# Performance work log

Hardware: AMD Instinct MI355X
Metric: run time of the kernel (lower is better)

The kernel has to match this reference:

```python
import jax, jax.numpy as jnp
import numpy as np

B, S, E = 2, 8192, 128


def setup_inputs() -> dict:
    key = jax.random.key(0)
    ks = jax.random.split(key, 7)
    sc = 1.0 / np.sqrt(E)
    return {
        "x": jax.random.normal(ks[0], (B, S, E), dtype=jnp.float32),
        "Wq": jax.random.normal(ks[1], (E, E), dtype=jnp.float32) * sc,
        "bq": jax.random.normal(ks[2], (E,), dtype=jnp.float32) * 0.01,
        "Wk": jax.random.normal(ks[3], (E, E), dtype=jnp.float32) * sc,
        "bk": jax.random.normal(ks[4], (E,), dtype=jnp.float32) * 0.01,
        "Wv": jax.random.normal(ks[5], (E, E), dtype=jnp.float32) * sc,
        "bv": jax.random.normal(ks[6], (E,), dtype=jnp.float32) * 0.01,
    }


def reference(x, Wq, bq, Wk, bk, Wv, bv):
    # x: [B, S, E]. Conv1d(k=1) == per-slice linear: out[b,s,o] = sum_e W[o,e] x[b,s,e] + b[o]
    embed_dim = x.shape[-1]
    Q = jnp.einsum("bse,oe->bso", x, Wq) + bq  # [B, S, E]
    K = jnp.einsum("bse,oe->bso", x, Wk) + bk
    V = jnp.einsum("bse,oe->bso", x, Wv) + bv
    scores = jnp.einsum("bsd,btd->bst", Q, K) / jnp.sqrt(
        jnp.asarray(embed_dim, dtype=x.dtype)
    )  # [B, S, S]
    A = jax.nn.softmax(scores, axis=-1)
    # torch: out = bmm(V^T_as[B,E,S], A^T)[.transpose] == sum_t A[b,s,t] V[b,t,e]
    out = jnp.einsum("bst,bte->bse", A, V)  # [B, S, E]
    return out
```

## Files before the change

kernel.cpp:

```cpp
#include <hip/hip_runtime.h>
#include <math.h>

#define NB 2
#define NS 8192
#define NE 128
#define NROWS (NB * NS)

typedef __attribute__((ext_vector_type(8))) short s8v;
typedef __attribute__((ext_vector_type(16))) float fx16;
typedef __attribute__((ext_vector_type(2))) unsigned int u2v;
typedef __attribute__((address_space(1))) const unsigned char as1c;
typedef __attribute__((address_space(3))) unsigned char as3t;

static __device__ __forceinline__ unsigned int pkbf(float a, float b) {
    unsigned int ua = __float_as_uint(a), ub = __float_as_uint(b);
    ua += 0x7FFFu + ((ua >> 16) & 1u);
    ub += 0x7FFFu + ((ub >> 16) & 1u);
    return (ua >> 16) | (ub & 0xFFFF0000u);
}

static __device__ __forceinline__ unsigned int cvtpk(float a, float b) {
    unsigned int r;
    asm("v_cvt_pk_bf16_f32 %0, %1, %2" : "=v"(r) : "v"(a), "v"(b));
    return r;
}

__global__ __launch_bounds__(256, 2)
void qkv_kernel(const float* __restrict__ x,
                const float* __restrict__ Wq, const float* __restrict__ bq,
                const float* __restrict__ Wk, const float* __restrict__ bk,
                const float* __restrict__ Wv, const float* __restrict__ bv,
                unsigned short* __restrict__ qkv)
{
    __shared__ unsigned short WhL[64 * 136];
    __shared__ unsigned short WlL[64 * 136];

    const int t    = threadIdx.x;
    const int rblk = blockIdx.x * 128;
    const int mat  = blockIdx.y;
    const int o0   = blockIdx.z * 64;

    const float* W    = (mat == 0) ? Wq : (mat == 1) ? Wk : Wv;
    const float* bias = (mat == 0) ? bq : (mat == 1) ? bk : bv;
    unsigned short* out = qkv + (size_t)mat * NROWS * NE;
    const float osc = (mat == 0) ? 0.1275174460620886f : 1.0f;

    {
        const int r = t >> 2, cg = (t & 3) * 32;
        #pragma unroll
        for (int j = 0; j < 4; ++j) {
            const float* wp = &W[(size_t)(o0 + r) * NE + cg + j * 8];
            float4 a = *(const float4*)wp;
            float4 b = *(const float4*)(wp + 4);
            unsigned int h0 = pkbf(a.x, a.y), h1 = pkbf(a.z, a.w);
            unsigned int h2 = pkbf(b.x, b.y), h3 = pkbf(b.z, b.w);
            *(uint4*)&WhL[r * 136 + cg + j * 8] = make_uint4(h0, h1, h2, h3);
            float l0 = a.x - __uint_as_float(h0 << 16);
            float l1 = a.y - __uint_as_float(h0 & 0xFFFF0000u);
            float l2 = a.z - __uint_as_float(h1 << 16);
            float l3 = a.w - __uint_as_float(h1 & 0xFFFF0000u);
            float l4 = b.x - __uint_as_float(h2 << 16);
            float l5 = b.y - __uint_as_float(h2 & 0xFFFF0000u);
            float l6 = b.z - __uint_as_float(h3 << 16);
            float l7 = b.w - __uint_as_float(h3 & 0xFFFF0000u);
            *(uint4*)&WlL[r * 136 + cg + j * 8] =
                make_uint4(pkbf(l0, l1), pkbf(l2, l3), pkbf(l4, l5), pkbf(l6, l7));
        }
    }
    __syncthreads();

    const int w = t >> 6, lane = t & 63, lq = lane & 31, h = lane >> 5;
    const int rw = rblk + w * 32;

    s8v xhf[8], xlf[8];
    #pragma unroll
    for (int s = 0; s < 8; ++s) {
        const float* xp = &x[(size_t)(rw + lq) * NE + s * 16 + h * 8];
        float4 a = *(const float4*)xp;
        float4 b = *(const float4*)(xp + 4);
        unsigned int h0 = pkbf(a.x, a.y), h1 = pkbf(a.z, a.w);
        unsigned int h2 = pkbf(b.x, b.y), h3 = pkbf(b.z, b.w);
        float l0 = a.x - __uint_as_float(h0 << 16);
        float l1 = a.y - __uint_as_float(h0 & 0xFFFF0000u);
        float l2 = a.z - __uint_as_float(h1 << 16);
        float l3 = a.w - __uint_as_float(h1 & 0xFFFF0000u);
        float l4 = b.x - __uint_as_float(h2 << 16);
        float l5 = b.y - __uint_as_float(h2 & 0xFFFF0000u);
        float l6 = b.z - __uint_as_float(h3 << 16);
        float l7 = b.w - __uint_as_float(h3 & 0xFFFF0000u);
        union { uint4 u; s8v v; } H, L;
        H.u = make_uint4(h0, h1, h2, h3);
        L.u = make_uint4(pkbf(l0, l1), pkbf(l2, l3), pkbf(l4, l5), pkbf(l6, l7));
        xhf[s] = H.v;
        xlf[s] = L.v;
    }

    fx16 acc[2];
    #pragma unroll
    for (int ot = 0; ot < 2; ++ot)
        #pragma unroll
        for (int i = 0; i < 16; ++i) acc[ot][i] = 0.f;

    #pragma unroll
    for (int s = 0; s < 8; ++s) {
        #pragma unroll
        for (int ot = 0; ot < 2; ++ot) {
            s8v wh = *(const s8v*)&WhL[(ot * 32 + lq) * 136 + s * 16 + h * 8];
            s8v wl = *(const s8v*)&WlL[(ot * 32 + lq) * 136 + s * 16 + h * 8];
            if (mat != 2) {
                acc[ot] = __builtin_amdgcn_mfma_f32_32x32x16_bf16(wh, xhf[s], acc[ot], 0, 0, 0);
                acc[ot] = __builtin_amdgcn_mfma_f32_32x32x16_bf16(wh, xlf[s], acc[ot], 0, 0, 0);
                acc[ot] = __builtin_amdgcn_mfma_f32_32x32x16_bf16(wl, xhf[s], acc[ot], 0, 0, 0);
            } else {
                acc[ot] = __builtin_amdgcn_mfma_f32_32x32x16_bf16(xhf[s], wh, acc[ot], 0, 0, 0);
                acc[ot] = __builtin_amdgcn_mfma_f32_32x32x16_bf16(xlf[s], wh, acc[ot], 0, 0, 0);
                acc[ot] = __builtin_amdgcn_mfma_f32_32x32x16_bf16(xhf[s], wl, acc[ot], 0, 0, 0);
            }
        }
    }

    if (mat != 2) {
        const size_t rbase = (size_t)(rw + lq) * NE;
        #pragma unroll
        for (int ot = 0; ot < 2; ++ot)
            #pragma unroll
            for (int g = 0; g < 4; ++g) {
                int ob = o0 + ot * 32 + 4 * h + 8 * g;
                float4 bb = *(const float4*)&bias[ob];
                float v0 = (acc[ot][4 * g + 0] + bb.x) * osc;
                float v1 = (acc[ot][4 * g + 1] + bb.y) * osc;
                float v2 = (acc[ot][4 * g + 2] + bb.z) * osc;
                float v3 = (acc[ot][4 * g + 3] + bb.w) * osc;
                *(uint2*)&out[rbase + ob] = make_uint2(pkbf(v0, v1), pkbf(v2, v3));
            }
    } else {
        const int bb_ = rw >> 13, kb = (rw & (NS - 1)) + 4 * h;
        #pragma unroll
        for (int ot = 0; ot < 2; ++ot) {
            int o = o0 + ot * 32 + lq;
            float bv = bias[o];
            size_t obase = ((size_t)(bb_ * NE + o) << 13) + kb;
            #pragma unroll
            for (int g = 0; g < 4; ++g) {
                float v0 = acc[ot][4 * g + 0] + bv;
                float v1 = acc[ot][4 * g + 1] + bv;
                float v2 = acc[ot][4 * g + 2] + bv;
                float v3 = acc[ot][4 * g + 3] + bv;
                *(uint2*)&out[obase + 8 * g] = make_uint2(pkbf(v0, v1), pkbf(v2, v3));
            }
        }
    }
}

__global__ __launch_bounds__(256, 2)
void attn_kernel(const unsigned short* __restrict__ qkv,
                 _Float16* __restrict__ pd,
                 _Float16* __restrict__ pw,
                 float* __restrict__ ml)
{
    __shared__ unsigned short kbuf[2][64 * 128];
    __shared__ unsigned short vbuf[2][64 * 128];

    const int t  = threadIdx.x;
    const int id = blockIdx.x;
    const int ks = id & 3;
    const int b  = (id >> 2) & 1;
    const int T  = id >> 3;

    const unsigned short* Qg = qkv;
    const unsigned short* Kg = qkv + (size_t)NROWS * NE;
    const unsigned short* Vb = qkv + (size_t)2 * NROWS * NE + ((size_t)b << 20);

    const int w = t >> 6, lane = t & 63, lq = lane & 31, h = lane >> 5;
    const int qbw = b * NS + T * 128 + w * 32;
    const size_t kvb = (size_t)b * NS * NE;
    const int kq0 = ks * 2048;

    s8v qf[8];
    #pragma unroll
    for (int s = 0; s < 8; ++s)
        qf[s] = *(const s8v*)(Qg + (size_t)(qbw + lq) * NE + s * 16 + h * 8);

    fx16 acc[4];
    #pragma unroll
    for (int dt = 0; dt < 4; ++dt)
        #pragma unroll
        for (int i = 0; i < 16; ++i) acc[dt][i] = 0.f;

    float l = 0.f;

    const unsigned short* gptr[8];
    if (w < 2) {
        #pragma unroll
        for (int j = 0; j < 8; ++j) {
            int i = 8 * w + j;
            int keyl = 4 * i + (lane >> 4);
            int c = (lane & 15) ^ (keyl & 7);
            gptr[j] = Kg + kvb + (size_t)(kq0 + keyl) * NE + c * 8;
        }
    } else {
        #pragma unroll
        for (int j = 0; j < 8; ++j) {
            int i = 8 * (w - 2) + j;
            int d = 8 * i + (lane >> 3);
            int g = (lane & 7) ^ (d & 7);
            gptr[j] = Vb + ((size_t)d << 13) + kq0 + g * 8;
        }
    }
    const int gstride = (w < 2) ? 64 * NE : 64;

    auto stage = [&](int bufi) {
        if (w < 2) {
            #pragma unroll
            for (int j = 0; j < 8; ++j) {
                __builtin_amdgcn_global_load_lds((as1c*)gptr[j],
                    (as3t*)&kbuf[bufi][(8 * w + j) * 512], 16, 0, 0);
                gptr[j] += gstride;
            }
        } else {
            #pragma unroll
            for (int j = 0; j < 8; ++j) {
                __builtin_amdgcn_global_load_lds((as1c*)gptr[j],
                    (as3t*)&vbuf[bufi][(8 * (w - 2) + j) * 512], 16, 0, 0);
                gptr[j] += gstride;
            }
        }
    };

    stage(0);
    __syncthreads();

#define PEX(i) (st2[(i) >> 4][(i) & 15])
    int buf = 0;
    const int swz = (lq & 7) * 8;

    for (int r = 0; r < 32; ++r) {
        if (r < 31) stage(buf ^ 1);

        fx16 st2[2];
        #pragma unroll
        for (int mt = 0; mt < 2; ++mt)
            #pragma unroll
            for (int i = 0; i < 16; ++i) st2[mt][i] = 0.f;
        __builtin_amdgcn_s_setprio(1);
        #pragma unroll
        for (int s = 0; s < 8; ++s) {
            int co = ((s * 2 + h) * 8) ^ swz;
            s8v a0 = *(const s8v*)&kbuf[buf][lq * 128 + co];
            s8v a1 = *(const s8v*)&kbuf[buf][(32 + lq) * 128 + co];
            st2[0] = __builtin_amdgcn_mfma_f32_32x32x16_bf16(a0, qf[s], st2[0], 0, 0, 0);
            st2[1] = __builtin_amdgcn_mfma_f32_32x32x16_bf16(a1, qf[s], st2[1], 0, 0, 0);
        }
        __builtin_amdgcn_s_setprio(0);

        float a0s = 0.f, a1s = 0.f, a2s = 0.f, a3s = 0.f;
        #pragma unroll
        for (int i = 0; i < 32; i += 4) {
            PEX(i)     = __builtin_amdgcn_exp2f(PEX(i));
            PEX(i + 1) = __builtin_amdgcn_exp2f(PEX(i + 1));
            PEX(i + 2) = __builtin_amdgcn_exp2f(PEX(i + 2));
            PEX(i + 3) = __builtin_amdgcn_exp2f(PEX(i + 3));
            a0s += PEX(i); a1s += PEX(i + 1); a2s += PEX(i + 2); a3s += PEX(i + 3);
        }
        float lsum = (a0s + a1s) + (a2s + a3s);
        lsum += __shfl_xor(lsum, 32);
        l += lsum;

        #pragma unroll
        for (int s2 = 0; s2 < 4; ++s2) {
            unsigned int P0 = cvtpk(PEX(s2 * 8 + 0), PEX(s2 * 8 + 1));
            unsigned int P1 = cvtpk(PEX(s2 * 8 + 2), PEX(s2 * 8 + 3));
            unsigned int P2 = cvtpk(PEX(s2 * 8 + 4), PEX(s2 * 8 + 5));
            unsigned int P3 = cvtpk(PEX(s2 * 8 + 6), PEX(s2 * 8 + 7));
            u2v r02 = __builtin_amdgcn_permlane32_swap(P0, P2, false, false);
            u2v r13 = __builtin_amdgcn_permlane32_swap(P1, P3, false, false);
            union { unsigned int u[4]; s8v v; } pf;
            pf.u[0] = r02.x;
            pf.u[1] = r13.x;
            pf.u[2] = r02.y;
            pf.u[3] = r13.y;
            int go = ((s2 * 2 + h) * 8) ^ swz;
            __builtin_amdgcn_s_setprio(1);
            #pragma unroll
            for (int dt = 0; dt < 4; ++dt) {
                s8v vf = *(const s8v*)&vbuf[buf][(lq + 32 * dt) * 64 + go];
                acc[dt] = __builtin_amdgcn_mfma_f32_32x32x16_bf16(pf.v, vf, acc[dt], 0, 0, 0);
            }
            __builtin_amdgcn_s_setprio(0);
        }

        __syncthreads();
        buf ^= 1;
    }
#undef PEX

    if (lane < 32)
        ml[(size_t)(qbw + lq) * 4 + ks] = l;

    float invl = 1.0f / l;
    _Float16* P = (ks < 2) ? pd : pw;
    const int slot = (ks & 1) * 128;
    #pragma unroll
    for (int rg = 0; rg < 16; ++rg) {
        int row = (rg & 3) + 8 * (rg >> 2) + 4 * h;
        float sc = __shfl(invl, row);
        size_t rb = (size_t)(qbw + row) * 256 + slot;
        #pragma unroll
        for (int dt = 0; dt < 4; ++dt)
            P[rb + lq + 32 * dt] = (_Float16)(acc[dt][rg] * sc);
    }
}

__global__ __launch_bounds__(256, 2)
void merge_kernel(const _Float16* __restrict__ pw,
                  const float* __restrict__ ml,
                  float* __restrict__ outp)
{
    const int gi = blockIdx.x * 256 + threadIdx.x;
    const int q = gi >> 4, d0 = (gi & 15) * 8;
    const _Float16* pd = (const _Float16*)outp;

    uint4 u0 = *(const uint4*)&pd[(size_t)q * 256 + d0];
    uint4 u1 = *(const uint4*)&pd[(size_t)q * 256 + 128 + d0];
    uint4 u2 = *(const uint4*)&pw[(size_t)q * 256 + d0];
    uint4 u3 = *(const uint4*)&pw[(size_t)q * 256 + 128 + d0];
    float l0 = ml[q * 4 + 0], l1 = ml[q * 4 + 1];
    float l2 = ml[q * 4 + 2], l3 = ml[q * 4 + 3];

    float inv = 1.f / (l0 + l1 + l2 + l3);
    float a0 = l0 * inv, a1 = l1 * inv, a2 = l2 * inv, a3 = l3 * inv;

    union { uint4 u; _Float16 hh[8]; } c0, c1, c2, c3;
    c0.u = u0; c1.u = u1; c2.u = u2; c3.u = u3;
    float ov[8];
    #pragma unroll
    for (int e = 0; e < 8; ++e)
        ov[e] = (float)c0.hh[e] * a0 + (float)c1.hh[e] * a1 +
                (float)c2.hh[e] * a2 + (float)c3.hh[e] * a3;

    *(float4*)&outp[(size_t)q * 128 + d0]     = *(float4*)&ov[0];
    *(float4*)&outp[(size_t)q * 128 + d0 + 4] = *(float4*)&ov[4];
}

extern "C" void kernel_launch(void* const* d_in, const int* in_sizes, int n_in,
                              void* d_out, int out_size, void* d_ws, size_t ws_size,
                              hipStream_t stream)
{
    const float* x  = (const float*)d_in[0];
    const float* Wq = (const float*)d_in[1];
    const float* bq = (const float*)d_in[2];
    const float* Wk = (const float*)d_in[3];
    const float* bk = (const float*)d_in[4];
    const float* Wv = (const float*)d_in[5];
    const float* bv = (const float*)d_in[6];
    float* out = (float*)d_out;

    unsigned char* ws = (unsigned char*)d_ws;
    unsigned short* qkv = (unsigned short*)ws;
    _Float16* pw = (_Float16*)(ws + (size_t)3 * NROWS * NE * 2);
    float* mlp = (float*)(ws + (size_t)3 * NROWS * NE * 2
                             + (size_t)NROWS * 256 * 2);

    dim3 g1(NROWS / 128, 3, 2);
    qkv_kernel<<<g1, 256, 0, stream>>>(x, Wq, bq, Wk, bk, Wv, bv, qkv);

    attn_kernel<<<512, 256, 0, stream>>>(qkv, (_Float16*)d_out, pw, mlp);
    merge_kernel<<<1024, 256, 0, stream>>>(pw, mlp, out);
}
```

Baseline: 163.7 us.

## Split attention keys eight ways with 512-thread blocks covering 256 queries

The attention kernel now uses 8 waves per block covering 256 query rows, and splits the key range eight ways instead of four. Each block loops over 1024 keys in 16 double-buffered stages, with four waves loading K and four loading V. The merge kernel now combines eight partial outputs and normalizers, so partial-output traffic grows. The launch bound asks for 4 such blocks per CU, which may force heavy register limits or spills, while the 64KB of LDS per block already caps how many blocks fit.

Result: slower. 204.9 us (+25.2%).

```diff
diff --git a/kernel.cpp b/kernel.cpp
--- a/kernel.cpp
+++ b/kernel.cpp
@@ -152,7 +152,7 @@
     }
 }
 
-__global__ __launch_bounds__(256, 2)
+__global__ __launch_bounds__(512, 4)
 void attn_kernel(const unsigned short* __restrict__ qkv,
                  _Float16* __restrict__ pd,
                  _Float16* __restrict__ pw,
@@ -163,18 +163,18 @@
 
     const int t  = threadIdx.x;
     const int id = blockIdx.x;
-    const int ks = id & 3;
-    const int b  = (id >> 2) & 1;
-    const int T  = id >> 3;
+    const int ks = id & 7;
+    const int b  = (id >> 3) & 1;
+    const int T  = id >> 4;
 
     const unsigned short* Qg = qkv;
     const unsigned short* Kg = qkv + (size_t)NROWS * NE;
     const unsigned short* Vb = qkv + (size_t)2 * NROWS * NE + ((size_t)b << 20);
 
     const int w = t >> 6, lane = t & 63, lq = lane & 31, h = lane >> 5;
-    const int qbw = b * NS + T * 128 + w * 32;
+    const int qbw = b * NS + T * 256 + w * 32;
     const size_t kvb = (size_t)b * NS * NE;
-    const int kq0 = ks * 2048;
+    const int kq0 = ks * 1024;
 
     s8v qf[8];
     #pragma unroll
@@ -189,39 +189,39 @@
 
     float l = 0.f;
 
-    const unsigned short* gptr[8];
-    if (w < 2) {
-        #pragma unroll
-        for (int j = 0; j < 8; ++j) {
-            int i = 8 * w + j;
+    const unsigned short* gptr[4];
+    if (w < 4) {
+        #pragma unroll
+        for (int j = 0; j < 4; ++j) {
+            int i = 4 * w + j;
             int keyl = 4 * i + (lane >> 4);
             int c = (lane & 15) ^ (keyl & 7);
             gptr[j] = Kg + kvb + (size_t)(kq0 + keyl) * NE + c * 8;
         }
     } else {
         #pragma unroll
-        for (int j = 0; j < 8; ++j) {
-            int i = 8 * (w - 2) + j;
+        for (int j = 0; j < 4; ++j) {
+            int i = 4 * (w - 4) + j;
             int d = 8 * i + (lane >> 3);
             int g = (lane & 7) ^ (d & 7);
             gptr[j] = Vb + ((size_t)d << 13) + kq0 + g * 8;
         }
     }
-    const int gstride = (w < 2) ? 64 * NE : 64;
+    const int gstride = (w < 4) ? 64 * NE : 64;
 
     auto stage = [&](int bufi) {
-        if (w < 2) {
-            #pragma unroll
-            for (int j = 0; j < 8; ++j) {
+        if (w < 4) {
+            #pragma unroll
+            for (int j = 0; j < 4; ++j) {
                 __builtin_amdgcn_global_load_lds((as1c*)gptr[j],
-                    (as3t*)&kbuf[bufi][(8 * w + j) * 512], 16, 0, 0);
+                    (as3t*)&kbuf[bufi][(4 * w + j) * 512], 16, 0, 0);
                 gptr[j] += gstride;
             }
         } else {
             #pragma unroll
-            for (int j = 0; j < 8; ++j) {
+            for (int j = 0; j < 4; ++j) {
                 __builtin_amdgcn_global_load_lds((as1c*)gptr[j],
-                    (as3t*)&vbuf[bufi][(8 * (w - 2) + j) * 512], 16, 0, 0);
+                    (as3t*)&vbuf[bufi][(4 * (w - 4) + j) * 512], 16, 0, 0);
                 gptr[j] += gstride;
             }
         }
@@ -234,8 +234,8 @@
     int buf = 0;
     const int swz = (lq & 7) * 8;
 
-    for (int r = 0; r < 32; ++r) {
-        if (r < 31) stage(buf ^ 1);
+    for (int r = 0; r < 16; ++r) {
+        if (r < 15) stage(buf ^ 1);
 
         fx16 st2[2];
         #pragma unroll
@@ -295,16 +295,18 @@
 #undef PEX
 
     if (lane < 32)
-        ml[(size_t)(qbw + lq) * 4 + ks] = l;
+        ml[(size_t)(qbw + lq) * 8 + ks] = l;
 
     float invl = 1.0f / l;
-    _Float16* P = (ks < 2) ? pd : pw;
-    const int slot = (ks & 1) * 128;
+    _Float16* P;
+    int rstride, slot;
+    if (ks < 2) { P = pd; rstride = 256; slot = ks * 128; }
+    else        { P = pw; rstride = 768; slot = (ks - 2) * 128; }
     #pragma unroll
     for (int rg = 0; rg < 16; ++rg) {
         int row = (rg & 3) + 8 * (rg >> 2) + 4 * h;
         float sc = __shfl(invl, row);
-        size_t rb = (size_t)(qbw + row) * 256 + slot;
+        size_t rb = (size_t)(qbw + row) * rstride + slot;
         #pragma unroll
         for (int dt = 0; dt < 4; ++dt)
             P[rb + lq + 32 * dt] = (_Float16)(acc[dt][rg] * sc);
@@ -320,23 +322,28 @@
     const int q = gi >> 4, d0 = (gi & 15) * 8;
     const _Float16* pd = (const _Float16*)outp;
 
-    uint4 u0 = *(const uint4*)&pd[(size_t)q * 256 + d0];
-    uint4 u1 = *(const uint4*)&pd[(size_t)q * 256 + 128 + d0];
-    uint4 u2 = *(const uint4*)&pw[(size_t)q * 256 + d0];
-    uint4 u3 = *(const uint4*)&pw[(size_t)q * 256 + 128 + d0];
-    float l0 = ml[q * 4 + 0], l1 = ml[q * 4 + 1];
-    float l2 = ml[q * 4 + 2], l3 = ml[q * 4 + 3];
-
-    float inv = 1.f / (l0 + l1 + l2 + l3);
-    float a0 = l0 * inv, a1 = l1 * inv, a2 = l2 * inv, a3 = l3 * inv;
-
-    union { uint4 u; _Float16 hh[8]; } c0, c1, c2, c3;
-    c0.u = u0; c1.u = u1; c2.u = u2; c3.u = u3;
+    union { uint4 u; _Float16 hh[8]; } c[8];
+    c[0].u = *(const uint4*)&pd[(size_t)q * 256 + d0];
+    c[1].u = *(const uint4*)&pd[(size_t)q * 256 + 128 + d0];
+    #pragma unroll
+    for (int p = 0; p < 6; ++p)
+        c[2 + p].u = *(const uint4*)&pw[(size_t)q * 768 + p * 128 + d0];
+
+    float4 la = *(const float4*)&ml[q * 8];
+    float4 lb = *(const float4*)&ml[q * 8 + 4];
+    float inv = 1.f / ((la.x + la.y + la.z + la.w) + (lb.x + lb.y + lb.z + lb.w));
+    float wg[8] = { la.x * inv, la.y * inv, la.z * inv, la.w * inv,
+                    lb.x * inv, lb.y * inv, lb.z * inv, lb.w * inv };
+
     float ov[8];
     #pragma unroll
-    for (int e = 0; e < 8; ++e)
-        ov[e] = (float)c0.hh[e] * a0 + (float)c1.hh[e] * a1 +
-                (float)c2.hh[e] * a2 + (float)c3.hh[e] * a3;
+    for (int e = 0; e < 8; ++e) {
+        float s = 0.f;
+        #pragma unroll
+        for (int p = 0; p < 8; ++p)
+            s += (float)c[p].hh[e] * wg[p];
+        ov[e] = s;
+    }
 
     *(float4*)&outp[(size_t)q * 128 + d0]     = *(float4*)&ov[0];
     *(float4*)&outp[(size_t)q * 128 + d0 + 4] = *(float4*)&ov[4];
@@ -359,11 +366,11 @@
     unsigned short* qkv = (unsigned short*)ws;
     _Float16* pw = (_Float16*)(ws + (size_t)3 * NROWS * NE * 2);
     float* mlp = (float*)(ws + (size_t)3 * NROWS * NE * 2
-                             + (size_t)NROWS * 256 * 2);
+                             + (size_t)NROWS * 768 * 2);
 
     dim3 g1(NROWS / 128, 3, 2);
     qkv_kernel<<<g1, 256, 0, stream>>>(x, Wq, bq, Wk, bk, Wv, bv, qkv);
 
-    attn_kernel<<<512, 256, 0, stream>>>(qkv, (_Float16*)d_out, pw, mlp);
+    attn_kernel<<<512, 512, 0, stream>>>(qkv, (_Float16*)d_out, pw, mlp);
     merge_kernel<<<1024, 256, 0, stream>>>(pw, mlp, out);
 }
```

## Process two 32-row query tiles per wave to double K/V reuse

Applied to the files above, without the earlier changes.

Each wave now handles 64 query rows (two 32-row MFMA tiles) instead of 32, so every K and V fragment read from LDS feeds two MFMAs. The block covers 256 queries, the grid is halved to 256 blocks, and launch bounds drop to one block per SM to make room for the doubled accumulators and Q fragments. This cuts K/V global staging and LDS traffic per query at the cost of higher register pressure, lower occupancy, and only 256 blocks to spread across the CUs.

Measured after the change: 170.3 us. 1.04x slower.

```diff
diff --git a/kernel.cpp b/kernel.cpp
--- a/kernel.cpp
+++ b/kernel.cpp
@@ -152,7 +152,7 @@
     }
 }
 
-__global__ __launch_bounds__(256, 2)
+__global__ __launch_bounds__(256, 1)
 void attn_kernel(const unsigned short* __restrict__ qkv,
                  _Float16* __restrict__ pd,
                  _Float16* __restrict__ pw,
@@ -172,22 +172,24 @@
     const unsigned short* Vb = qkv + (size_t)2 * NROWS * NE + ((size_t)b << 20);
 
     const int w = t >> 6, lane = t & 63, lq = lane & 31, h = lane >> 5;
-    const int qbw = b * NS + T * 128 + w * 32;
+    const int qbw = b * NS + T * 256 + w * 64;
     const size_t kvb = (size_t)b * NS * NE;
     const int kq0 = ks * 2048;
 
-    s8v qf[8];
-    #pragma unroll
-    for (int s = 0; s < 8; ++s)
-        qf[s] = *(const s8v*)(Qg + (size_t)(qbw + lq) * NE + s * 16 + h * 8);
-
-    fx16 acc[4];
+    s8v qfA[8], qfB[8];
+    #pragma unroll
+    for (int s = 0; s < 8; ++s) {
+        qfA[s] = *(const s8v*)(Qg + (size_t)(qbw + lq) * NE + s * 16 + h * 8);
+        qfB[s] = *(const s8v*)(Qg + (size_t)(qbw + 32 + lq) * NE + s * 16 + h * 8);
+    }
+
+    fx16 accA[4], accB[4];
     #pragma unroll
     for (int dt = 0; dt < 4; ++dt)
         #pragma unroll
-        for (int i = 0; i < 16; ++i) acc[dt][i] = 0.f;
-
-    float l = 0.f;
+        for (int i = 0; i < 16; ++i) { accA[dt][i] = 0.f; accB[dt][i] = 0.f; }
+
+    float lA = 0.f, lB = 0.f;
 
     const unsigned short* gptr[8];
     if (w < 2) {
@@ -230,61 +232,72 @@
     stage(0);
     __syncthreads();
 
-#define PEX(i) (st2[(i) >> 4][(i) & 15])
+#define PEXA(i) (stA[(i) >> 4][(i) & 15])
+#define PEXB(i) (stB[(i) >> 4][(i) & 15])
     int buf = 0;
     const int swz = (lq & 7) * 8;
 
     for (int r = 0; r < 32; ++r) {
         if (r < 31) stage(buf ^ 1);
 
-        fx16 st2[2];
+        fx16 stA[2], stB[2];
         #pragma unroll
         for (int mt = 0; mt < 2; ++mt)
             #pragma unroll
-            for (int i = 0; i < 16; ++i) st2[mt][i] = 0.f;
+            for (int i = 0; i < 16; ++i) { stA[mt][i] = 0.f; stB[mt][i] = 0.f; }
         __builtin_amdgcn_s_setprio(1);
         #pragma unroll
         for (int s = 0; s < 8; ++s) {
             int co = ((s * 2 + h) * 8) ^ swz;
             s8v a0 = *(const s8v*)&kbuf[buf][lq * 128 + co];
             s8v a1 = *(const s8v*)&kbuf[buf][(32 + lq) * 128 + co];
-            st2[0] = __builtin_amdgcn_mfma_f32_32x32x16_bf16(a0, qf[s], st2[0], 0, 0, 0);
-            st2[1] = __builtin_amdgcn_mfma_f32_32x32x16_bf16(a1, qf[s], st2[1], 0, 0, 0);
+            stA[0] = __builtin_amdgcn_mfma_f32_32x32x16_bf16(a0, qfA[s], stA[0], 0, 0, 0);
+            stB[0] = __builtin_amdgcn_mfma_f32_32x32x16_bf16(a0, qfB[s], stB[0], 0, 0, 0);
+            stA[1] = __builtin_amdgcn_mfma_f32_32x32x16_bf16(a1, qfA[s], stA[1], 0, 0, 0);
+            stB[1] = __builtin_amdgcn_mfma_f32_32x32x16_bf16(a1, qfB[s], stB[1], 0, 0, 0);
         }
         __builtin_amdgcn_s_setprio(0);
 
-        float a0s = 0.f, a1s = 0.f, a2s = 0.f, a3s = 0.f;
-        #pragma unroll
-        for (int i = 0; i < 32; i += 4) {
-            PEX(i)     = __builtin_amdgcn_exp2f(PEX(i));
-            PEX(i + 1) = __builtin_amdgcn_exp2f(PEX(i + 1));
-            PEX(i + 2) = __builtin_amdgcn_exp2f(PEX(i + 2));
-            PEX(i + 3) = __builtin_amdgcn_exp2f(PEX(i + 3));
-            a0s += PEX(i); a1s += PEX(i + 1); a2s += PEX(i + 2); a3s += PEX(i + 3);
-        }
-        float lsum = (a0s + a1s) + (a2s + a3s);
-        lsum += __shfl_xor(lsum, 32);
-        l += lsum;
+        float aA0 = 0.f, aA1 = 0.f, aB0 = 0.f, aB1 = 0.f;
+        #pragma unroll
+        for (int i = 0; i < 32; i += 2) {
+            PEXA(i)     = __builtin_amdgcn_exp2f(PEXA(i));
+            PEXB(i)     = __builtin_amdgcn_exp2f(PEXB(i));
+            PEXA(i + 1) = __builtin_amdgcn_exp2f(PEXA(i + 1));
+            PEXB(i + 1) = __builtin_amdgcn_exp2f(PEXB(i + 1));
+            aA0 += PEXA(i); aA1 += PEXA(i + 1);
+            aB0 += PEXB(i); aB1 += PEXB(i + 1);
+        }
+        float lsA = aA0 + aA1, lsB = aB0 + aB1;
+        lsA += __shfl_xor(lsA, 32);
+        lsB += __shfl_xor(lsB, 32);
+        lA += lsA;
+        lB += lsB;
 
         #pragma unroll
         for (int s2 = 0; s2 < 4; ++s2) {
-            unsigned int P0 = cvtpk(PEX(s2 * 8 + 0), PEX(s2 * 8 + 1));
-            unsigned int P1 = cvtpk(PEX(s2 * 8 + 2), PEX(s2 * 8 + 3));
-            unsigned int P2 = cvtpk(PEX(s2 * 8 + 4), PEX(s2 * 8 + 5));
-            unsigned int P3 = cvtpk(PEX(s2 * 8 + 6), PEX(s2 * 8 + 7));
-            u2v r02 = __builtin_amdgcn_permlane32_swap(P0, P2, false, false);
-            u2v r13 = __builtin_amdgcn_permlane32_swap(P1, P3, false, false);
-            union { unsigned int u[4]; s8v v; } pf;
-            pf.u[0] = r02.x;
-            pf.u[1] = r13.x;
-            pf.u[2] = r02.y;
-            pf.u[3] = r13.y;
+            unsigned int A0 = cvtpk(PEXA(s2 * 8 + 0), PEXA(s2 * 8 + 1));
+            unsigned int A1 = cvtpk(PEXA(s2 * 8 + 2), PEXA(s2 * 8 + 3));
+            unsigned int A2 = cvtpk(PEXA(s2 * 8 + 4), PEXA(s2 * 8 + 5));
+            unsigned int A3 = cvtpk(PEXA(s2 * 8 + 6), PEXA(s2 * 8 + 7));
+            u2v a02 = __builtin_amdgcn_permlane32_swap(A0, A2, false, false);
+            u2v a13 = __builtin_amdgcn_permlane32_swap(A1, A3, false, false);
+            unsigned int B0 = cvtpk(PEXB(s2 * 8 + 0), PEXB(s2 * 8 + 1));
+            unsigned int B1 = cvtpk(PEXB(s2 * 8 + 2), PEXB(s2 * 8 + 3));
+            unsigned int B2 = cvtpk(PEXB(s2 * 8 + 4), PEXB(s2 * 8 + 5));
+            unsigned int B3 = cvtpk(PEXB(s2 * 8 + 6), PEXB(s2 * 8 + 7));
+            u2v b02 = __builtin_amdgcn_permlane32_swap(B0, B2, false, false);
+            u2v b13 = __builtin_amdgcn_permlane32_swap(B1, B3, false, false);
+            union { unsigned int u[4]; s8v v; } pfA, pfB;
+            pfA.u[0] = a02.x; pfA.u[1] = a13.x; pfA.u[2] = a02.y; pfA.u[3] = a13.y;
+            pfB.u[0] = b02.x; pfB.u[1] = b13.x; pfB.u[2] = b02.y; pfB.u[3] = b13.y;
             int go = ((s2 * 2 + h) * 8) ^ swz;
             __builtin_amdgcn_s_setprio(1);
             #pragma unroll
             for (int dt = 0; dt < 4; ++dt) {
                 s8v vf = *(const s8v*)&vbuf[buf][(lq + 32 * dt) * 64 + go];
-                acc[dt] = __builtin_amdgcn_mfma_f32_32x32x16_bf16(pf.v, vf, acc[dt], 0, 0, 0);
+                accA[dt] = __builtin_amdgcn_mfma_f32_32x32x16_bf16(pfA.v, vf, accA[dt], 0, 0, 0);
+                accB[dt] = __builtin_amdgcn_mfma_f32_32x32x16_bf16(pfB.v, vf, accB[dt], 0, 0, 0);
             }
             __builtin_amdgcn_s_setprio(0);
         }
@@ -292,22 +305,29 @@
         __syncthreads();
         buf ^= 1;
     }
-#undef PEX
-
-    if (lane < 32)
-        ml[(size_t)(qbw + lq) * 4 + ks] = l;
-
-    float invl = 1.0f / l;
+#undef PEXA
+#undef PEXB
+
+    if (lane < 32) {
+        ml[(size_t)(qbw + lq) * 4 + ks]      = lA;
+        ml[(size_t)(qbw + 32 + lq) * 4 + ks] = lB;
+    }
+
+    float invlA = 1.0f / lA, invlB = 1.0f / lB;
     _Float16* P = (ks < 2) ? pd : pw;
     const int slot = (ks & 1) * 128;
     #pragma unroll
     for (int rg = 0; rg < 16; ++rg) {
         int row = (rg & 3) + 8 * (rg >> 2) + 4 * h;
-        float sc = __shfl(invl, row);
-        size_t rb = (size_t)(qbw + row) * 256 + slot;
-        #pragma unroll
-        for (int dt = 0; dt < 4; ++dt)
-            P[rb + lq + 32 * dt] = (_Float16)(acc[dt][rg] * sc);
+        float scA = __shfl(invlA, row);
+        float scB = __shfl(invlB, row);
+        size_t rbA = (size_t)(qbw + row) * 256 + slot;
+        size_t rbB = (size_t)(qbw + 32 + row) * 256 + slot;
+        #pragma unroll
+        for (int dt = 0; dt < 4; ++dt) {
+            P[rbA + lq + 32 * dt] = (_Float16)(accA[dt][rg] * scA);
+            P[rbB + lq + 32 * dt] = (_Float16)(accB[dt][rg] * scB);
+        }
     }
 }
 
@@ -364,6 +384,6 @@
     dim3 g1(NROWS / 128, 3, 2);
     qkv_kernel<<<g1, 256, 0, stream>>>(x, Wq, bq, Wk, bk, Wv, bv, qkv);
 
-    attn_kernel<<<512, 256, 0, stream>>>(qkv, (_Float16*)d_out, pw, mlp);
+    attn_kernel<<<256, 256, 0, stream>>>(qkv, (_Float16*)d_out, pw, mlp);
     merge_kernel<<<1024, 256, 0, stream>>>(pw, mlp, out);
 }
```

## Precompute bf16 hi/lo splits in separate kernel and DMA weights into LDS

Applied to the files above, without the earlier changes.

Adds a split_kernel that converts x and the three weight matrices into bf16 high/low pairs once, writing the weights in an XOR-swizzled layout. The QKV kernel then loads the pre-split x fragments directly and uses global_load_lds to copy the weights into unpadded, swizzled LDS, rather than redoing the conversion in each of its 6 blocks per row tile. The intent is to remove repeated fp32-to-bf16 split work and the padded LDS stores, and to raise the occupancy hint. The cost is an extra kernel launch plus a workspace round trip for x (write and reread of two bf16 copies), which may offset the savings.

Result: no change. 165.2 us (+0.9%).

```diff
diff --git a/kernel.cpp b/kernel.cpp
--- a/kernel.cpp
+++ b/kernel.cpp
@@ -25,49 +25,83 @@
     return r;
 }
 
-__global__ __launch_bounds__(256, 2)
-void qkv_kernel(const float* __restrict__ x,
-                const float* __restrict__ Wq, const float* __restrict__ bq,
-                const float* __restrict__ Wk, const float* __restrict__ bk,
-                const float* __restrict__ Wv, const float* __restrict__ bv,
+static __device__ __forceinline__ void split8(const float* p, uint4& H, uint4& L) {
+    float4 a = *(const float4*)p;
+    float4 b = *(const float4*)(p + 4);
+    unsigned int h0 = cvtpk(a.x, a.y), h1 = cvtpk(a.z, a.w);
+    unsigned int h2 = cvtpk(b.x, b.y), h3 = cvtpk(b.z, b.w);
+    H = make_uint4(h0, h1, h2, h3);
+    float l0 = a.x - __uint_as_float(h0 << 16);
+    float l1 = a.y - __uint_as_float(h0 & 0xFFFF0000u);
+    float l2 = a.z - __uint_as_float(h1 << 16);
+    float l3 = a.w - __uint_as_float(h1 & 0xFFFF0000u);
+    float l4 = b.x - __uint_as_float(h2 << 16);
+    float l5 = b.y - __uint_as_float(h2 & 0xFFFF0000u);
+    float l6 = b.z - __uint_as_float(h3 << 16);
+    float l7 = b.w - __uint_as_float(h3 & 0xFFFF0000u);
+    L = make_uint4(cvtpk(l0, l1), cvtpk(l2, l3), cvtpk(l4, l5), cvtpk(l6, l7));
+}
+
+__global__ __launch_bounds__(256, 4)
+void split_kernel(const float* __restrict__ x,
+                  const float* __restrict__ Wq, const float* __restrict__ Wk,
+                  const float* __restrict__ Wv,
+                  unsigned short* __restrict__ xh, unsigned short* __restrict__ xl,
+                  unsigned short* __restrict__ WhS, unsigned short* __restrict__ WlS)
+{
+    const int bid = blockIdx.x;
+    if (bid < 1024) {
+        const int i = (bid * 256 + threadIdx.x) * 8;
+        uint4 H, L;
+        split8(&x[i], H, L);
+        *(uint4*)&xh[i] = H;
+        *(uint4*)&xl[i] = L;
+    } else {
+        const int tid = (bid - 1024) * 256 + threadIdx.x;
+        const int mat = tid >> 11;
+        const int rem = tid & 2047;
+        const int r = rem >> 4, g = rem & 15;
+        const float* W = (mat == 0) ? Wq : (mat == 1) ? Wk : Wv;
+        uint4 H, L;
+        split8(&W[r * 128 + g * 8], H, L);
+        const int gs = g ^ (r & 7);
+        *(uint4*)&WhS[mat * 16384 + r * 128 + gs * 8] = H;
+        *(uint4*)&WlS[mat * 16384 + r * 128 + gs * 8] = L;
+    }
+}
+
+__global__ __launch_bounds__(256, 3)
+void qkv_kernel(const unsigned short* __restrict__ xh,
+                const unsigned short* __restrict__ xl,
+                const unsigned short* __restrict__ WhS,
+                const unsigned short* __restrict__ WlS,
+                const float* __restrict__ bq, const float* __restrict__ bk,
+                const float* __restrict__ bv,
                 unsigned short* __restrict__ qkv)
 {
-    __shared__ unsigned short WhL[64 * 136];
-    __shared__ unsigned short WlL[64 * 136];
+    __shared__ unsigned short WhL[64 * 128];
+    __shared__ unsigned short WlL[64 * 128];
 
     const int t    = threadIdx.x;
     const int rblk = blockIdx.x * 128;
     const int mat  = blockIdx.y;
     const int o0   = blockIdx.z * 64;
 
-    const float* W    = (mat == 0) ? Wq : (mat == 1) ? Wk : Wv;
     const float* bias = (mat == 0) ? bq : (mat == 1) ? bk : bv;
     unsigned short* out = qkv + (size_t)mat * NROWS * NE;
     const float osc = (mat == 0) ? 0.1275174460620886f : 1.0f;
 
     {
-        const int r = t >> 2, cg = (t & 3) * 32;
-        #pragma unroll
-        for (int j = 0; j < 4; ++j) {
-            const float* wp = &W[(size_t)(o0 + r) * NE + cg + j * 8];
-            float4 a = *(const float4*)wp;
-            float4 b = *(const float4*)(wp + 4);
-            unsigned int h0 = pkbf(a.x, a.y), h1 = pkbf(a.z, a.w);
-            unsigned int h2 = pkbf(b.x, b.y), h3 = pkbf(b.z, b.w);
-            *(uint4*)&WhL[r * 136 + cg + j * 8] = make_uint4(h0, h1, h2, h3);
-            float l0 = a.x - __uint_as_float(h0 << 16);
-            float l1 = a.y - __uint_as_float(h0 & 0xFFFF0000u);
-            float l2 = a.z - __uint_as_float(h1 << 16);
-            float l3 = a.w - __uint_as_float(h1 & 0xFFFF0000u);
-            float l4 = b.x - __uint_as_float(h2 << 16);
-            float l5 = b.y - __uint_as_float(h2 & 0xFFFF0000u);
-            float l6 = b.z - __uint_as_float(h3 << 16);
-            float l7 = b.w - __uint_as_float(h3 & 0xFFFF0000u);
-            *(uint4*)&WlL[r * 136 + cg + j * 8] =
-                make_uint4(pkbf(l0, l1), pkbf(l2, l3), pkbf(l4, l5), pkbf(l6, l7));
-        }
-    }
-    __syncthreads();
+        const unsigned short* hsrc = WhS + mat * 16384 + o0 * 128;
+        const unsigned short* lsrc = WlS + mat * 16384 + o0 * 128;
+        #pragma unroll
+        for (int p = 0; p < 4; ++p) {
+            __builtin_amdgcn_global_load_lds((as1c*)(hsrc + p * 2048 + t * 8),
+                (as3t*)&WhL[p * 2048 + t * 8], 16, 0, 0);
+            __builtin_amdgcn_global_load_lds((as1c*)(lsrc + p * 2048 + t * 8),
+                (as3t*)&WlL[p * 2048 + t * 8], 16, 0, 0);
+        }
+    }
 
     const int w = t >> 6, lane = t & 63, lq = lane & 31, h = lane >> 5;
     const int rw = rblk + w * 32;
@@ -75,25 +109,11 @@
     s8v xhf[8], xlf[8];
     #pragma unroll
     for (int s = 0; s < 8; ++s) {
-        const float* xp = &x[(size_t)(rw + lq) * NE + s * 16 + h * 8];
-        float4 a = *(const float4*)xp;
-        float4 b = *(const float4*)(xp + 4);
-        unsigned int h0 = pkbf(a.x, a.y), h1 = pkbf(a.z, a.w);
-        unsigned int h2 = pkbf(b.x, b.y), h3 = pkbf(b.z, b.w);
-        float l0 = a.x - __uint_as_float(h0 << 16);
-        float l1 = a.y - __uint_as_float(h0 & 0xFFFF0000u);
-        float l2 = a.z - __uint_as_float(h1 << 16);
-        float l3 = a.w - __uint_as_float(h1 & 0xFFFF0000u);
-        float l4 = b.x - __uint_as_float(h2 << 16);
-        float l5 = b.y - __uint_as_float(h2 & 0xFFFF0000u);
-        float l6 = b.z - __uint_as_float(h3 << 16);
-        float l7 = b.w - __uint_as_float(h3 & 0xFFFF0000u);
-        union { uint4 u; s8v v; } H, L;
-        H.u = make_uint4(h0, h1, h2, h3);
-        L.u = make_uint4(pkbf(l0, l1), pkbf(l2, l3), pkbf(l4, l5), pkbf(l6, l7));
-        xhf[s] = H.v;
-        xlf[s] = L.v;
-    }
+        xhf[s] = *(const s8v*)(xh + (size_t)(rw + lq) * NE + s * 16 + h * 8);
+        xlf[s] = *(const s8v*)(xl + (size_t)(rw + lq) * NE + s * 16 + h * 8);
+    }
+
+    __syncthreads();
 
     fx16 acc[2];
     #pragma unroll
@@ -105,8 +125,9 @@
     for (int s = 0; s < 8; ++s) {
         #pragma unroll
         for (int ot = 0; ot < 2; ++ot) {
-            s8v wh = *(const s8v*)&WhL[(ot * 32 + lq) * 136 + s * 16 + h * 8];
-            s8v wl = *(const s8v*)&WlL[(ot * 32 + lq) * 136 + s * 16 + h * 8];
+            const int co = ((s * 2 + h) ^ (lq & 7)) * 8;
+            s8v wh = *(const s8v*)&WhL[(ot * 32 + lq) * 128 + co];
+            s8v wl = *(const s8v*)&WlL[(ot * 32 + lq) * 128 + co];
             if (mat != 2) {
                 acc[ot] = __builtin_amdgcn_mfma_f32_32x32x16_bf16(wh, xhf[s], acc[ot], 0, 0, 0);
                 acc[ot] = __builtin_amdgcn_mfma_f32_32x32x16_bf16(wh, xlf[s], acc[ot], 0, 0, 0);
@@ -138,14 +159,14 @@
         #pragma unroll
         for (int ot = 0; ot < 2; ++ot) {
             int o = o0 + ot * 32 + lq;
-            float bv = bias[o];
+            float bv_ = bias[o];
             size_t obase = ((size_t)(bb_ * NE + o) << 13) + kb;
             #pragma unroll
             for (int g = 0; g < 4; ++g) {
-                float v0 = acc[ot][4 * g + 0] + bv;
-                float v1 = acc[ot][4 * g + 1] + bv;
-                float v2 = acc[ot][4 * g + 2] + bv;
-                float v3 = acc[ot][4 * g + 3] + bv;
+                float v0 = acc[ot][4 * g + 0] + bv_;
+                float v1 = acc[ot][4 * g + 1] + bv_;
+                float v2 = acc[ot][4 * g + 2] + bv_;
+                float v3 = acc[ot][4 * g + 3] + bv_;
                 *(uint2*)&out[obase + 8 * g] = make_uint2(pkbf(v0, v1), pkbf(v2, v3));
             }
         }
@@ -360,9 +381,17 @@
     _Float16* pw = (_Float16*)(ws + (size_t)3 * NROWS * NE * 2);
     float* mlp = (float*)(ws + (size_t)3 * NROWS * NE * 2
                              + (size_t)NROWS * 256 * 2);
+    unsigned char* ws2 = ws + (size_t)3 * NROWS * NE * 2
+                            + (size_t)NROWS * 256 * 2 + (size_t)NROWS * 16;
+    unsigned short* xh  = (unsigned short*)ws2;
+    unsigned short* xl  = xh + (size_t)NROWS * NE;
+    unsigned short* WhS = xl + (size_t)NROWS * NE;
+    unsigned short* WlS = WhS + 3 * NE * NE;
+
+    split_kernel<<<1048, 256, 0, stream>>>(x, Wq, Wk, Wv, xh, xl, WhS, WlS);
 
     dim3 g1(NROWS / 128, 3, 2);
-    qkv_kernel<<<g1, 256, 0, stream>>>(x, Wq, bq, Wk, bk, Wv, bv, qkv);
+    qkv_kernel<<<g1, 256, 0, stream>>>(xh, xl, WhS, WlS, bq, bk, bv, qkv);
 
     attn_kernel<<<512, 256, 0, stream>>>(qkv, (_Float16*)d_out, pw, mlp);
     merge_kernel<<<1024, 256, 0, stream>>>(pw, mlp, out);
```
